# Kernel tuning notes

Hardware: AMD Instinct MI355X
Metric: run time of the kernel (lower is better)

## Reference

```python
import jax, jax.numpy as jnp
import numpy as np


def _laplacian_kernel(x, z, bandwidth):
    x_sq = jnp.sum(x * x, axis=-1, keepdims=True)          # [N, 1]
    z_sq = jnp.sum(z * z, axis=-1)[None, :]                # [1, M]
    d2 = x_sq + z_sq - 2.0 * jnp.einsum('nd,md->nm', x, z)  # [N, M]
    d = jnp.sqrt(jnp.maximum(d2, 0.0))
    return jnp.exp(-d / bandwidth)


def setup_inputs() -> dict:
    key = jax.random.key(0)
    k1, k2, k3 = jax.random.split(key, 3)
    N, M, D, Y = 8192, 20000, 1024, 256
    batch = jax.random.normal(k1, (N, D), dtype=jnp.float32)
    centers = jax.random.normal(k2, (M, D), dtype=jnp.float32)
    weight = jax.random.normal(k3, (M, Y), dtype=jnp.float32) * 0.02
    return {"batch": batch, "centers": centers, "weight": weight, "bandwidth": 10}


def reference(batch, centers, weight, bandwidth):
    kmat = _laplacian_kernel(batch, centers, float(bandwidth))  # [N, M]
    pred = kmat @ weight                                        # [N, Y]
    return pred
```

## Files before the change

kernel.cpp:

```cpp
#include <hip/hip_runtime.h>
#include <stdint.h>

#define N_ROWS 8192
#define D_DIM  1024
#define M_CENT 20000
#define M_PAD  20224
#define M_TILES 79
#define Y_DIM  256
#define BM 64
#define BN 256
#define BK 64
#define MSPLIT 8
#define TILES_PER_SPLIT 10
#define LDSP_STRIDE 264

typedef __attribute__((ext_vector_type(4))) float  f32x4;
typedef __attribute__((ext_vector_type(8))) __bf16 bf16x8;

__device__ __forceinline__ unsigned short f2bf(float f) {
    union { float f; unsigned u; } v; v.f = f;
    unsigned u = v.u;
    u += 0x7FFFu + ((u >> 16) & 1u);
    return (unsigned short)(u >> 16);
}

__device__ __forceinline__ void gll16(void* lds, const void* g) {
    __builtin_amdgcn_global_load_lds(
        (const __attribute__((address_space(1))) void*)g,
        (__attribute__((address_space(3))) void*)lds, 16, 0, 0);
}

__global__ void cast_rows_kernel(const float* __restrict__ src,
                                 unsigned short* __restrict__ dst,
                                 float* __restrict__ sq, int nrows_valid) {
    int row = blockIdx.x;
    int t = threadIdx.x;
    float s = 0.f;
    if (row < nrows_valid) {
        float4 v = ((const float4*)(src + (size_t)row * D_DIM))[t];
        s = v.x * v.x + v.y * v.y + v.z * v.z + v.w * v.w;
        ushort4 o;
        o.x = f2bf(v.x); o.y = f2bf(v.y); o.z = f2bf(v.z); o.w = f2bf(v.w);
        ((ushort4*)(dst + (size_t)row * D_DIM))[t] = o;
    } else {
        ((ushort4*)(dst + (size_t)row * D_DIM))[t] = make_ushort4(0, 0, 0, 0);
    }
    __shared__ float red[4];
    for (int off = 32; off; off >>= 1) s += __shfl_down(s, off, 64);
    if ((t & 63) == 0) red[t >> 6] = s;
    __syncthreads();
    if (t == 0) sq[row] = red[0] + red[1] + red[2] + red[3];
}

__global__ void cast_wT_kernel(const float* __restrict__ w,
                               unsigned short* __restrict__ wT) {
    __shared__ float tile[32][33];
    int k0 = blockIdx.x * 32;
    int y0 = blockIdx.y * 32;
    int tx = threadIdx.x & 31;
    int ty = threadIdx.x >> 5;
    #pragma unroll
    for (int i = 0; i < 4; ++i) {
        int k = k0 + ty + i * 8;
        float v = (k < M_CENT) ? w[(size_t)k * Y_DIM + y0 + tx] : 0.f;
        tile[tx][ty + i * 8] = v;
    }
    __syncthreads();
    #pragma unroll
    for (int i = 0; i < 4; ++i) {
        int yl = ty + i * 8;
        wT[(size_t)(y0 + yl) * M_PAD + k0 + tx] = f2bf(tile[yl][tx]);
    }
}

__global__ void __launch_bounds__(256, 2)
fused_kernel(const unsigned short* __restrict__ Xb,
             const unsigned short* __restrict__ Zb,
             const unsigned short* __restrict__ WbT,
             const float* __restrict__ xsq,
             const float* __restrict__ zsq,
             const int* __restrict__ bwp,
             float* __restrict__ out) {
    __shared__ union {
        struct {
            unsigned short x[BM * BK];
            unsigned short z[BN * BK];
        } s1;
        unsigned short p[BM * LDSP_STRIDE];
    } lds;
    __shared__ float lds_xsq[BM];
    __shared__ float lds_zsq[BN];

    const int t    = threadIdx.x;
    const int wave = t >> 6;
    const int lane = t & 63;
    const int quad = lane >> 4;
    const int l16  = lane & 15;
    const int cx   = l16 & 7;

    const int row0 = blockIdx.x * BM;
    int mt = blockIdx.y * TILES_PER_SPLIT;
    int mt_end = mt + TILES_PER_SPLIT;
    if (mt_end > M_TILES) mt_end = M_TILES;

    int bwi = *bwp;
    float bw;
    if (bwi > 0 && bwi < 1000000) bw = (float)bwi;
    else { union { int i; float f; } u; u.i = bwi; bw = u.f; }
    const float inv_bw = 1.0f / bw;

    if (t < BM) lds_xsq[t] = xsq[row0 + t];

    const f32x4 vzero = {0.f, 0.f, 0.f, 0.f};
    f32x4 Oacc[16];
    #pragma unroll
    for (int i = 0; i < 16; ++i) Oacc[i] = vzero;

    for (; mt < mt_end; ++mt) {
        __syncthreads();

        const int m0 = mt * BN;
        lds_zsq[t] = zsq[m0 + t];

        f32x4 S[16];
        #pragma unroll
        for (int i = 0; i < 16; ++i) S[i] = vzero;

        for (int kc = 0; kc < D_DIM / BK; ++kc) {
            const int kbase = kc * BK;
            #pragma unroll
            for (int i = 0; i < 2; ++i) {
                int lin = t + i * 256;
                int row = lin >> 3, c = lin & 7;
                gll16(&lds.s1.x[lin * 8],
                      Xb + (size_t)(row0 + row) * D_DIM + kbase + ((c ^ (row & 7)) * 8));
            }
            #pragma unroll
            for (int i = 0; i < 8; ++i) {
                int lin = t + i * 256;
                int row = lin >> 3, c = lin & 7;
                gll16(&lds.s1.z[lin * 8],
                      Zb + (size_t)(m0 + row) * D_DIM + kbase + ((c ^ (row & 7)) * 8));
            }
            __syncthreads();
            #pragma unroll
            for (int kt = 0; kt < 2; ++kt) {
                const int sw = ((kt * 4 + quad) ^ cx) * 8;
                bf16x8 a[4], b[4];
                #pragma unroll
                for (int it = 0; it < 4; ++it)
                    a[it] = *(const bf16x8*)&lds.s1.x[(it * 16 + l16) * BK + sw];
                #pragma unroll
                for (int jt = 0; jt < 4; ++jt)
                    b[jt] = *(const bf16x8*)&lds.s1.z[(wave * 64 + jt * 16 + l16) * BK + sw];
                #pragma unroll
                for (int it = 0; it < 4; ++it)
                    #pragma unroll
                    for (int jt = 0; jt < 4; ++jt)
                        S[it * 4 + jt] = __builtin_amdgcn_mfma_f32_16x16x32_bf16(
                            a[it], b[jt], S[it * 4 + jt], 0, 0, 0);
            }
            __syncthreads();
        }

        #pragma unroll
        for (int it = 0; it < 4; ++it) {
            #pragma unroll
            for (int jt = 0; jt < 4; ++jt) {
                f32x4 s4 = S[it * 4 + jt];
                const int col = wave * 64 + jt * 16 + l16;
                const float zq = lds_zsq[col];
                #pragma unroll
                for (int r = 0; r < 4; ++r) {
                    const int row = it * 16 + quad * 4 + r;
                    float d2 = lds_xsq[row] + zq - 2.0f * s4[r];
                    d2 = fmaxf(d2, 0.f);
                    float p = __expf(-sqrtf(d2) * inv_bw);
                    lds.p[row * LDSP_STRIDE + col] = f2bf(p);
                }
            }
        }
        __syncthreads();

        #pragma unroll
        for (int ks = 0; ks < 8; ++ks) {
            const int koff = ks * 32 + quad * 8;
            bf16x8 a[4], b[4];
            #pragma unroll
            for (int rt = 0; rt < 4; ++rt)
                a[rt] = *(const bf16x8*)&lds.p[(rt * 16 + l16) * LDSP_STRIDE + koff];
            #pragma unroll
            for (int ct = 0; ct < 4; ++ct) {
                const int y = wave * 64 + ct * 16 + l16;
                b[ct] = *(const bf16x8*)(WbT + (size_t)y * M_PAD + m0 + koff);
            }
            #pragma unroll
            for (int rt = 0; rt < 4; ++rt)
                #pragma unroll
                for (int ct = 0; ct < 4; ++ct)
                    Oacc[rt * 4 + ct] = __builtin_amdgcn_mfma_f32_16x16x32_bf16(
                        a[rt], b[ct], Oacc[rt * 4 + ct], 0, 0, 0);
        }
    }

    #pragma unroll
    for (int rt = 0; rt < 4; ++rt) {
        #pragma unroll
        for (int ct = 0; ct < 4; ++ct) {
            f32x4 v = Oacc[rt * 4 + ct];
            const int y = wave * 64 + ct * 16 + l16;
            #pragma unroll
            for (int r = 0; r < 4; ++r) {
                const int row = row0 + rt * 16 + quad * 4 + r;
                atomicAdd(&out[(size_t)row * Y_DIM + y], v[r]);
            }
        }
    }
}

extern "C" void kernel_launch(void* const* d_in, const int* in_sizes, int n_in,
                              void* d_out, int out_size, void* d_ws, size_t ws_size,
                              hipStream_t stream) {
    const float* X = (const float*)d_in[0];
    const float* Z = (const float*)d_in[1];
    const float* W = (const float*)d_in[2];
    const int*  bw = (const int*)d_in[3];
    float* out = (float*)d_out;

    char* ws = (char*)d_ws;
    size_t off = 0;
    unsigned short* Xb  = (unsigned short*)(ws + off); off += (size_t)N_ROWS * D_DIM * 2;
    unsigned short* Zb  = (unsigned short*)(ws + off); off += (size_t)M_PAD * D_DIM * 2;
    unsigned short* WbT = (unsigned short*)(ws + off); off += (size_t)Y_DIM * M_PAD * 2;
    float* xsq = (float*)(ws + off); off += (size_t)N_ROWS * 4;
    float* zsq = (float*)(ws + off); off += (size_t)M_PAD * 4;

    hipMemsetAsync(d_out, 0, (size_t)out_size * sizeof(float), stream);
    cast_rows_kernel<<<N_ROWS, 256, 0, stream>>>(X, Xb, xsq, N_ROWS);
    cast_rows_kernel<<<M_PAD, 256, 0, stream>>>(Z, Zb, zsq, M_CENT);
    cast_wT_kernel<<<dim3(M_PAD / 32, Y_DIM / 32), 256, 0, stream>>>(W, WbT);
    fused_kernel<<<dim3(N_ROWS / BM, MSPLIT), 256, 0, stream>>>(Xb, Zb, WbT, xsq, zsq, bw, out);
}
```

Baseline: 747.4 us.

## Double-buffer X in LDS, stream Z directly to registers, remap grid for locality

Z tiles are now loaded straight from global memory into registers and prefetched one chunk ahead, and X tiles are double-buffered in LDS. This removes the large Z LDS staging and one barrier per K chunk. The M split drops from 8 to 4 on a 1D grid, and the block-index mapping is changed so blocks that share row tiles run close together, which also halves the atomic output traffic. MFMA sections are wrapped in s_setprio. In exchange the kernel holds many more VGPRs for the register prefetch, which may hurt occupancy, and launches fewer blocks.

```diff
diff --git a/kernel.cpp b/kernel.cpp
--- a/kernel.cpp
+++ b/kernel.cpp
@@ -10,8 +10,9 @@
 #define BM 64
 #define BN 256
 #define BK 64
-#define MSPLIT 8
-#define TILES_PER_SPLIT 10
+#define NCHUNK 16
+#define MSPLIT 4
+#define TILES_PER_SPLIT 20
 #define LDSP_STRIDE 264
 
 typedef __attribute__((ext_vector_type(4))) float  f32x4;
@@ -73,6 +74,49 @@
     }
 }
 
+
+#define STAGE_X(PAR, KBASE) do {                                              \
+    _Pragma("unroll")                                                         \
+    for (int i_ = 0; i_ < 2; ++i_) {                                          \
+        int lin_ = t + i_ * 256;                          \
+        int row_ = lin_ >> 3, c_ = lin_ & 7;                                  \
+        gll16(&lds_x[PAR][lin_ * 8],                                          \
+              Xb + (size_t)(row0 + row_) * D_DIM + (KBASE) +                  \
+                  ((c_ ^ (row_ & 7)) * 8));                                   \
+    } } while (0)
+
+#define LOAD_B(DST, M0, KBASE) do {                                           \
+    _Pragma("unroll")                                                         \
+    for (int kt_ = 0; kt_ < 2; ++kt_)                                         \
+        _Pragma("unroll")                                                     \
+        for (int jt_ = 0; jt_ < 4; ++jt_)                                     \
+            DST[kt_ * 4 + jt_] = *(const bf16x8*)(Zb +                        \
+                (size_t)((M0) + wave * 64 + jt_ * 16 + l16) * D_DIM +         \
+                (KBASE) + kt_ * 32 + quad * 8);                               \
+    } while (0)
+
+#define CHUNK(PAR, KBASE, M0N, KBN) do {                                      \
+    __syncthreads();                                                          \
+    LOAD_B(Bf[PAR ^ 1], M0N, KBN);                                            \
+    STAGE_X(PAR ^ 1, KBN);                                                    \
+    _Pragma("unroll")                                                         \
+    for (int kt_ = 0; kt_ < 2; ++kt_) {                                       \
+        bf16x8 a_[4];                                                         \
+        _Pragma("unroll")                                                     \
+        for (int it_ = 0; it_ < 4; ++it_)                                     \
+            a_[it_] = *(const bf16x8*)&lds_x[PAR][                            \
+                (it_ * 16 + l16) * BK + ((kt_ * 4 + quad) ^ cx) * 8];         \
+        __builtin_amdgcn_s_setprio(1);                                        \
+        _Pragma("unroll")                                                     \
+        for (int it_ = 0; it_ < 4; ++it_)                                     \
+            _Pragma("unroll")                                                 \
+            for (int jt_ = 0; jt_ < 4; ++jt_)                                 \
+                S[it_ * 4 + jt_] = __builtin_amdgcn_mfma_f32_16x16x32_bf16(   \
+                    a_[it_], Bf[PAR][kt_ * 4 + jt_], S[it_ * 4 + jt_],        \
+                    0, 0, 0);                                                 \
+        __builtin_amdgcn_s_setprio(0);                                        \
+    } } while (0)
+
 __global__ void __launch_bounds__(256, 2)
 fused_kernel(const unsigned short* __restrict__ Xb,
              const unsigned short* __restrict__ Zb,
@@ -81,15 +125,9 @@
              const float* __restrict__ zsq,
              const int* __restrict__ bwp,
              float* __restrict__ out) {
-    __shared__ union {
-        struct {
-            unsigned short x[BM * BK];
-            unsigned short z[BN * BK];
-        } s1;
-        unsigned short p[BM * LDSP_STRIDE];
-    } lds;
+    __shared__ unsigned short lds_x[2][BM * BK];
+    __shared__ unsigned short lds_p[BM * LDSP_STRIDE];
     __shared__ float lds_xsq[BM];
-    __shared__ float lds_zsq[BN];
 
     const int t    = threadIdx.x;
     const int wave = t >> 6;
@@ -98,8 +136,12 @@
     const int l16  = lane & 15;
     const int cx   = l16 & 7;
 
-    const int row0 = blockIdx.x * BM;
-    int mt = blockIdx.y * TILES_PER_SPLIT;
+    const int bid    = blockIdx.x;
+    const int ysplit = bid & 3;
+    const int xblk   = (bid >> 3) + 64 * ((bid >> 2) & 1);
+    const int row0   = xblk * BM;
+
+    int mt     = ysplit * TILES_PER_SPLIT;
     int mt_end = mt + TILES_PER_SPLIT;
     if (mt_end > M_TILES) mt_end = M_TILES;
 
@@ -116,51 +158,31 @@
     #pragma unroll
     for (int i = 0; i < 16; ++i) Oacc[i] = vzero;
 
+    bf16x8 Bf[2][8];
+
+    STAGE_X(0, 0);
+    LOAD_B(Bf[0], mt * BN, 0);
+
     for (; mt < mt_end; ++mt) {
-        __syncthreads();
-
         const int m0 = mt * BN;
-        lds_zsq[t] = zsq[m0 + t];
+        const int m0next = (mt + 1 < mt_end) ? m0 + BN : m0;
+
+        float zq[4];
+        #pragma unroll
+        for (int jt = 0; jt < 4; ++jt)
+            zq[jt] = zsq[m0 + wave * 64 + jt * 16 + l16];
 
         f32x4 S[16];
         #pragma unroll
         for (int i = 0; i < 16; ++i) S[i] = vzero;
 
-        for (int kc = 0; kc < D_DIM / BK; ++kc) {
-            const int kbase = kc * BK;
-            #pragma unroll
-            for (int i = 0; i < 2; ++i) {
-                int lin = t + i * 256;
-                int row = lin >> 3, c = lin & 7;
-                gll16(&lds.s1.x[lin * 8],
-                      Xb + (size_t)(row0 + row) * D_DIM + kbase + ((c ^ (row & 7)) * 8));
-            }
-            #pragma unroll
-            for (int i = 0; i < 8; ++i) {
-                int lin = t + i * 256;
-                int row = lin >> 3, c = lin & 7;
-                gll16(&lds.s1.z[lin * 8],
-                      Zb + (size_t)(m0 + row) * D_DIM + kbase + ((c ^ (row & 7)) * 8));
-            }
-            __syncthreads();
-            #pragma unroll
-            for (int kt = 0; kt < 2; ++kt) {
-                const int sw = ((kt * 4 + quad) ^ cx) * 8;
-                bf16x8 a[4], b[4];
-                #pragma unroll
-                for (int it = 0; it < 4; ++it)
-                    a[it] = *(const bf16x8*)&lds.s1.x[(it * 16 + l16) * BK + sw];
-                #pragma unroll
-                for (int jt = 0; jt < 4; ++jt)
-                    b[jt] = *(const bf16x8*)&lds.s1.z[(wave * 64 + jt * 16 + l16) * BK + sw];
-                #pragma unroll
-                for (int it = 0; it < 4; ++it)
-                    #pragma unroll
-                    for (int jt = 0; jt < 4; ++jt)
-                        S[it * 4 + jt] = __builtin_amdgcn_mfma_f32_16x16x32_bf16(
-                            a[it], b[jt], S[it * 4 + jt], 0, 0, 0);
-            }
-            __syncthreads();
+        #pragma unroll 1
+        for (int kc = 0; kc < NCHUNK; kc += 2) {
+            const int kb0 = kc * BK;
+            const int kb1 = kb0 + BK;
+            const bool last = (kc + 2 == NCHUNK);
+            CHUNK(0, kb0, m0, kb1);
+            CHUNK(1, kb1, last ? m0next : m0, last ? 0 : kb1 + BK);
         }
 
         #pragma unroll
@@ -169,14 +191,13 @@
             for (int jt = 0; jt < 4; ++jt) {
                 f32x4 s4 = S[it * 4 + jt];
                 const int col = wave * 64 + jt * 16 + l16;
-                const float zq = lds_zsq[col];
                 #pragma unroll
                 for (int r = 0; r < 4; ++r) {
                     const int row = it * 16 + quad * 4 + r;
-                    float d2 = lds_xsq[row] + zq - 2.0f * s4[r];
+                    float d2 = lds_xsq[row] + zq[jt] - 2.0f * s4[r];
                     d2 = fmaxf(d2, 0.f);
                     float p = __expf(-sqrtf(d2) * inv_bw);
-                    lds.p[row * LDSP_STRIDE + col] = f2bf(p);
+                    lds_p[row * LDSP_STRIDE + col] = f2bf(p);
                 }
             }
         }
@@ -188,18 +209,20 @@
             bf16x8 a[4], b[4];
             #pragma unroll
             for (int rt = 0; rt < 4; ++rt)
-                a[rt] = *(const bf16x8*)&lds.p[(rt * 16 + l16) * LDSP_STRIDE + koff];
+                a[rt] = *(const bf16x8*)&lds_p[(rt * 16 + l16) * LDSP_STRIDE + koff];
             #pragma unroll
             for (int ct = 0; ct < 4; ++ct) {
                 const int y = wave * 64 + ct * 16 + l16;
                 b[ct] = *(const bf16x8*)(WbT + (size_t)y * M_PAD + m0 + koff);
             }
+            __builtin_amdgcn_s_setprio(1);
             #pragma unroll
             for (int rt = 0; rt < 4; ++rt)
                 #pragma unroll
                 for (int ct = 0; ct < 4; ++ct)
                     Oacc[rt * 4 + ct] = __builtin_amdgcn_mfma_f32_16x16x32_bf16(
                         a[rt], b[ct], Oacc[rt * 4 + ct], 0, 0, 0);
+            __builtin_amdgcn_s_setprio(0);
         }
     }
 
@@ -239,5 +262,6 @@
     cast_rows_kernel<<<N_ROWS, 256, 0, stream>>>(X, Xb, xsq, N_ROWS);
     cast_rows_kernel<<<M_PAD, 256, 0, stream>>>(Z, Zb, zsq, M_CENT);
     cast_wT_kernel<<<dim3(M_PAD / 32, Y_DIM / 32), 256, 0, stream>>>(W, WbT);
-    fused_kernel<<<dim3(N_ROWS / BM, MSPLIT), 256, 0, stream>>>(Xb, Zb, WbT, xsq, zsq, bw, out);
-}
+    fused_kernel<<<dim3(MSPLIT * (N_ROWS / BM)), 256, 0, stream>>>(
+        Xb, Zb, WbT, xsq, zsq, bw, out);
+}
```

Measured after the change: 996.1 us. 33.3% more time.
